# Kernel tuning notes

Measured on AMD Instinct MI355X. Metric: run time of the kernel, lower is better.

## Reference

```python
import jax, jax.numpy as jnp
import numpy as np

NUM_HEADS = 16


def setup_inputs() -> dict:
    key = jax.random.key(0)
    ks = jax.random.split(key, 8)
    S, B, E, L, P = 512, 32, 1024, 16, 10
    query = jax.random.normal(ks[0], (S, B, E), dtype=jnp.float32)
    prompt_ids = jax.random.randint(ks[1], (B, 1), 0, P, dtype=jnp.int32)
    batch_weight = jax.random.uniform(ks[2], (B,), dtype=jnp.float32)
    # xavier_uniform-like init for in_proj_weight
    bound = float(np.sqrt(6.0 / (3 * E + E)))
    in_proj_weight = jax.random.uniform(ks[3], (3 * E, E), minval=-bound, maxval=bound, dtype=jnp.float32)
    in_proj_bias = jnp.zeros((3 * E,), dtype=jnp.float32)
    ob = float(np.sqrt(6.0 / (E + E)))
    out_proj_weight = jax.random.uniform(ks[4], (E, E), minval=-ob, maxval=ob, dtype=jnp.float32)
    out_proj_bias = jnp.zeros((E,), dtype=jnp.float32)
    # prefix_pool: K-half uniform(-1,1), V-half zeros (as in torch init)
    pk = jax.random.uniform(ks[5], (P, 1, L, E), minval=-1.0, maxval=1.0, dtype=jnp.float32)
    prefix_pool = jnp.concatenate([pk, jnp.zeros((P, 1, L, E), dtype=jnp.float32)], axis=1)
    return {
        "query": query,
        "prompt_ids": prompt_ids,
        "batch_weight": batch_weight,
        "in_proj_weight": in_proj_weight,
        "in_proj_bias": in_proj_bias,
        "out_proj_weight": out_proj_weight,
        "out_proj_bias": out_proj_bias,
        "prefix_pool": prefix_pool,
    }


def _sdpa(q, k, v, scale):
    # q: [B,H,S,D], k/v: [B,H,T,D]
    scores = jnp.einsum("bhsd,bhtd->bhst", q, k) * scale
    probs = jax.nn.softmax(scores, axis=-1)
    return jnp.einsum("bhst,bhtd->bhsd", probs, v)


def reference(query, prompt_ids, batch_weight, in_proj_weight, in_proj_bias,
              out_proj_weight, out_proj_bias, prefix_pool):
    S, B, E = query.shape
    H = NUM_HEADS
    D = E // H
    scale = 1.0 / jnp.sqrt(jnp.asarray(D, dtype=query.dtype))

    # packed in-projection (q is k is v)
    qkv = query @ in_proj_weight.T + in_proj_bias          # [S,B,3E]
    q, k, v = jnp.split(qkv, 3, axis=-1)
    to_bhsd = lambda t: t.reshape(S, B, H, D).transpose(1, 2, 0, 3)  # [B,H,S,D]
    q, k, v = to_bhsd(q), to_bhsd(k), to_bhsd(v)

    # main attention
    attn = _sdpa(q, k, v, scale)                           # [B,H,S,D]

    # prefix attention
    prefix = prefix_pool[prompt_ids[:, 0]]                 # [B,2,L,E]
    L = prefix.shape[2]
    pk = prefix[:, 0].reshape(B, L, H, D).transpose(0, 2, 1, 3)  # [B,H,L,D]
    pv = prefix[:, 1].reshape(B, L, H, D).transpose(0, 2, 1, 3)
    attn_prefix = _sdpa(q, pk, pv, scale)                  # [B,H,S,D]
    attn_prefix = attn_prefix * batch_weight[:, None, None, None]

    out = attn + attn_prefix
    out = out.transpose(2, 0, 1, 3).reshape(S, B, E)       # [S,B,E]
    out = out @ out_proj_weight.T + out_proj_bias
    return out
```

## Files before the change

kernel.cpp:

```cpp
#include <hip/hip_runtime.h>
#include <stdint.h>

typedef unsigned short u16;
typedef __attribute__((ext_vector_type(8))) __bf16 bf16x8;
typedef __attribute__((ext_vector_type(4))) float f32x4;
typedef __attribute__((ext_vector_type(8))) unsigned short ushort8;

__device__ __forceinline__ u16 f2bf(float f) {
  unsigned int u = __builtin_bit_cast(unsigned int, f);
  return (u16)((u + 0x7fffu + ((u >> 16) & 1u)) >> 16);
}

__device__ __forceinline__ float fexp2(float x) {
  float r;
  asm volatile("v_exp_f32 %0, %1" : "=v"(r) : "v"(x));
  return r;
}

__device__ __forceinline__ f32x4 mfma16(bf16x8 a, bf16x8 b, f32x4 c) {
  return __builtin_amdgcn_mfma_f32_16x16x32_bf16(a, b, c, 0, 0, 0);
}

__device__ __forceinline__ void gload_lds16(const void* g, void* l) {
  __builtin_amdgcn_global_load_lds((const __attribute__((address_space(1))) void*)g,
                                   (__attribute__((address_space(3))) void*)l,
                                   16, 0, 0);
}

#define KSCALE 0.18033688011112294f

__global__ void __launch_bounds__(256) cvt_all(
    const float* __restrict__ q, const float* __restrict__ w1,
    const float* __restrict__ w2, u16* __restrict__ qb,
    u16* __restrict__ w1b, u16* __restrict__ w2b) {
  int i = blockIdx.x * 256 + threadIdx.x;
  const float* src;
  u16* dst;
  int off;
  if (i < 4194304) {
    src = q; dst = qb; off = i;
  } else if (i < 4194304 + 786432) {
    src = w1; dst = w1b; off = i - 4194304;
  } else {
    src = w2; dst = w2b; off = i - 4980736;
  }
  float4 v = ((const float4*)src)[off];
  u16* d = dst + (size_t)off * 4;
  d[0] = f2bf(v.x); d[1] = f2bf(v.y); d[2] = f2bf(v.z); d[3] = f2bf(v.w);
}

#define LDV(p) (*(const bf16x8*)(p))
#define RD_LO(AS, C) { aL[0]=LDV(AS+aRow+(C)); aL[1]=LDV(AS+aRow+1024+(C)); \
                       aL[2]=LDV(AS+aRow+2048+(C)); aL[3]=LDV(AS+aRow+3072+(C)); }
#define RD_HI(AS, C) { aH[0]=LDV(AS+aRow+4096+(C)); aH[1]=LDV(AS+aRow+5120+(C)); \
                       aH[2]=LDV(AS+aRow+6144+(C)); aH[3]=LDV(AS+aRow+7168+(C)); }
#define RD_B(BS, R, C) { R[0]=LDV(BS+bRow+(C)); R[1]=LDV(BS+bRow+1024+(C)); \
                         R[2]=LDV(BS+bRow+2048+(C)); R[3]=LDV(BS+bRow+3072+(C)); }
#define STA(DST, Q, T) gload_lds16(baseA + (Q)*K64 + (size_t)(T)*64, (DST) + (Q)*4096 + stDst)
#define STB(DST, Q, T) gload_lds16(baseB + (Q)*K64 + (size_t)(T)*64, (DST) + (Q)*4096 + stDst)
#define MM_LO(BB) { _Pragma("unroll") for (int mi=0;mi<4;++mi) \
                    _Pragma("unroll") for (int ni=0;ni<4;++ni) \
                      acc[mi][ni]=mfma16(aL[mi],(BB)[ni],acc[mi][ni]); }
#define MM_HI(BB) { _Pragma("unroll") for (int mi=0;mi<4;++mi) \
                    _Pragma("unroll") for (int ni=0;ni<4;++ni) \
                      acc[mi+4][ni]=mfma16(aH[mi],(BB)[ni],acc[mi+4][ni]); }
#define VMW(N) asm volatile("s_waitcnt vmcnt(" #N ")" ::: "memory")
#define BAR() __builtin_amdgcn_s_barrier()
#define PRIO1() __builtin_amdgcn_s_setprio(1)
#define PRIO0() __builtin_amdgcn_s_setprio(0)
#define MFMA_PH(MM, BB) { PRIO1(); MM(BB); PRIO0(); }

template <int MODE>
__global__ void __launch_bounds__(512, 2) gemm8p(
    const u16* __restrict__ A, const u16* __restrict__ B,
    const float* __restrict__ bias, void* __restrict__ Cout,
    u16* __restrict__ q_out, u16* __restrict__ k_out, u16* __restrict__ v_out,
    int M, int N, int K) {
  __shared__ alignas(16) u16 As[2][16384];
  __shared__ alignas(16) u16 Bs[2][16384];

  const int tid = threadIdx.x;
  const int w = tid >> 6, l = tid & 63;
  const int wm = w >> 2, wn = w & 3;
  const long bm = (long)blockIdx.x * 256;
  const long bn = (long)blockIdx.y * 256;
  const int NT = K >> 6;
  const int NIT = NT >> 1;

  const int srow = w * 8 + (l >> 3);
  const int schk = ((l & 7) ^ (l >> 3)) * 8;
  const u16* baseA = A + (bm + srow) * (size_t)K + schk;
  const u16* baseB = B + (bn + srow) * (size_t)K + schk;
  const size_t K64 = (size_t)K * 64;
  const int stDst = w * 512;

  u16* const as0 = &As[0][0]; u16* const as1 = &As[1][0];
  u16* const bs0 = &Bs[0][0]; u16* const bs1 = &Bs[1][0];

  const int fr = l & 15, fkg = l >> 4;
  const int sw = (fr & 7) << 3;
  const int c0 = (fkg * 8) ^ sw;
  const int c1 = (32 + fkg * 8) ^ sw;
  const int aRow = (wm * 128 + fr) * 64;
  const int bRow = (wn * 64 + fr) * 64;

  f32x4 acc[8][4] = {};
  bf16x8 aL[4], aH[4], b0[4], b1[4];

  STB(bs0, 0, 0); STB(bs0, 1, 0);
  STB(bs0, 2, 0); STB(bs0, 3, 0);
  STA(as0, 0, 0); STA(as0, 2, 0);
  STA(as0, 1, 0); STA(as0, 3, 0);
  STB(bs1, 0, 1); STB(bs1, 1, 1);
  VMW(4); BAR();

  for (int it = 0; it < NIT - 1; ++it) {
    const int t1 = 2 * it + 1, t2 = 2 * it + 2, t3 = 2 * it + 3;
    RD_LO(as0, c0); RD_B(bs0, b0, c0);
    STB(bs1, 2, t1); STB(bs1, 3, t1);
    VMW(4); BAR(); MFMA_PH(MM_LO, b0); BAR();
    RD_HI(as0, c0);
    STA(as1, 0, t1); STA(as1, 2, t1);
    BAR(); MFMA_PH(MM_HI, b0); BAR();
    RD_LO(as0, c1); RD_B(bs0, b1, c1);
    STA(as1, 1, t1); STA(as1, 3, t1);
    BAR(); MFMA_PH(MM_LO, b1); BAR();
    RD_HI(as0, c1);
    STB(bs0, 0, t2); STB(bs0, 1, t2);
    VMW(4); BAR(); MFMA_PH(MM_HI, b1); BAR();
    RD_LO(as1, c0); RD_B(bs1, b0, c0);
    STB(bs0, 2, t2); STB(bs0, 3, t2);
    VMW(4); BAR(); MFMA_PH(MM_LO, b0); BAR();
    RD_HI(as1, c0);
    STA(as0, 0, t2); STA(as0, 2, t2);
    BAR(); MFMA_PH(MM_HI, b0); BAR();
    RD_LO(as1, c1); RD_B(bs1, b1, c1);
    STA(as0, 1, t2); STA(as0, 3, t2);
    BAR(); MFMA_PH(MM_LO, b1); BAR();
    RD_HI(as1, c1);
    STB(bs1, 0, t3); STB(bs1, 1, t3);
    VMW(4); BAR(); MFMA_PH(MM_HI, b1); BAR();
  }
  {
    const int t1 = NT - 1;
    RD_LO(as0, c0); RD_B(bs0, b0, c0);
    STB(bs1, 2, t1); STB(bs1, 3, t1);
    VMW(4); BAR(); MFMA_PH(MM_LO, b0); BAR();
    RD_HI(as0, c0);
    STA(as1, 0, t1); STA(as1, 2, t1);
    BAR(); MFMA_PH(MM_HI, b0); BAR();
    RD_LO(as0, c1); RD_B(bs0, b1, c1);
    STA(as1, 1, t1); STA(as1, 3, t1);
    BAR(); MFMA_PH(MM_LO, b1); BAR();
    RD_HI(as0, c1);
    VMW(2); BAR(); MFMA_PH(MM_HI, b1); BAR();
    RD_LO(as1, c0); RD_B(bs1, b0, c0);
    VMW(0); BAR(); MFMA_PH(MM_LO, b0); BAR();
    RD_HI(as1, c0);
    BAR(); MFMA_PH(MM_HI, b0); BAR();
    RD_LO(as1, c1); RD_B(bs1, b1, c1);
    BAR(); MFMA_PH(MM_LO, b1); BAR();
    RD_HI(as1, c1);
    BAR(); MFMA_PH(MM_HI, b1);
  }

  const int r0 = wm * 128 + ((l >> 4) << 2);
  const int cc0 = wn * 64 + (l & 15);
#pragma unroll
  for (int mi = 0; mi < 8; ++mi) {
#pragma unroll
    for (int j = 0; j < 4; ++j) {
      long r = bm + r0 + mi * 16 + j;
#pragma unroll
      for (int ni = 0; ni < 4; ++ni) {
        long c = bn + cc0 + ni * 16;
        float v = acc[mi][ni][j] + bias[c];
        if (MODE == 0) {
          ((float*)Cout)[r * N + c] = v;
        } else {
          int s = (int)(r >> 5), bb = (int)(r & 31);
          int sec = (int)(c >> 10), e = (int)(c & 1023);
          int hh = e >> 6, d = e & 63;
          if (sec == 0) v *= KSCALE;
          u16* dst = (sec == 0) ? q_out : (sec == 1) ? k_out : v_out;
          dst[(((size_t)(bb * 16 + hh) * 512 + s) * 64) + d] = f2bf(v);
        }
      }
    }
  }
}

__global__ void __launch_bounds__(1024, 4) attn_v4(
    const u16* __restrict__ Q, const u16* __restrict__ K, const u16* __restrict__ V,
    const float* __restrict__ prefix_pool, const int* __restrict__ prompt_ids,
    const float* __restrict__ batch_weight, u16* __restrict__ attn_out) {
  constexpr int E = 1024, L = 16;
  const int h = blockIdx.x, b = blockIdx.y;
  const int tid = threadIdx.x;
  const int wid = tid >> 6, lane = tid & 63;
  const int fr = lane & 15, fkg = lane >> 4;

  __shared__ alignas(16) u16 Ks[64 * 64];
  __shared__ alignas(16) u16 VTs[64 * 64];
  __shared__ alignas(16) u16 Ps[16][16 * 64];
  __shared__ alignas(16) u16 pKs[L * 64];
  __shared__ alignas(16) u16 pVTs[64 * 32];

  const size_t bh = (size_t)(b * 16 + h);
  const u16* Kbase = K + bh * 512 * 64;
  const u16* Vbase = V + bh * 512 * 64;
  const u16* Qbase = Q + bh * 512 * 64;
  const int q0 = wid * 32;

  const bool isK = (tid < 512);
  const int st = isK ? tid : tid - 512;
  const int srow = st >> 3;
  const int scol = (st & 7) * 8;
  const u16* sbase = (isK ? Kbase : Vbase) + srow * 64 + scol;

  ushort8 stgA, stgB;
  stgA = *(const ushort8*)(sbase);

  const int pid = prompt_ids[b];
  const float* pk = prefix_pool + ((size_t)pid * 2 * L) * E + h * 64;
  const float* pv = pk + (size_t)L * E;
  if (tid < 256) {
    int ll = tid >> 4, d0 = (tid & 15) * 4;
    float4 v = *(const float4*)(pk + (size_t)ll * E + d0);
    u16 t4[4] = {f2bf(v.x), f2bf(v.y), f2bf(v.z), f2bf(v.w)};
#pragma unroll
    for (int i = 0; i < 4; ++i)
      pKs[(ll * 64 + d0 + i) ^ ((ll & 7) << 3)] = t4[i];
  } else if (tid < 512) {
    int t = tid - 256;
    int d = t >> 2, kv0 = (t & 3) * 8;
#pragma unroll
    for (int i = 0; i < 8; ++i) {
      int kv = kv0 + i;
      float v = (kv < L) ? pv[(size_t)kv * E + d] : 0.f;
      pVTs[d * 32 + kv] = f2bf(v);
    }
  }

  bf16x8 qf[2][2];
#pragma unroll
  for (int mt = 0; mt < 2; ++mt) {
    int qrow = q0 + mt * 16 + fr;
    qf[mt][0] = *(const bf16x8*)(Qbase + qrow * 64 + fkg * 8);
    qf[mt][1] = *(const bf16x8*)(Qbase + qrow * 64 + 32 + fkg * 8);
  }

  float m2[2] = {-3e38f, -3e38f}, lsum[2] = {0.f, 0.f};
  f32x4 oacc[2][4] = {};
  u16* const pw = Ps[wid];
  const int psw = (fr & 7) << 3;

#define STAGE_WRITE(STG)                                                      \
  if (isK) {                                                                  \
    int e = (srow * 64 + scol) ^ ((srow & 7) << 3);                           \
    *(ushort8*)(Ks + e) = STG;                                                \
  } else {                                                                    \
    _Pragma("unroll") for (int i = 0; i < 8; ++i) {                           \
      int d = scol + i;                                                       \
      VTs[(d * 64 + srow) ^ ((d & 7) << 3)] = STG[i];                         \
    }                                                                         \
  }

#define COMPUTE(CC)                                                           \
  _Pragma("unroll") for (int mt = 0; mt < 2; ++mt) {                          \
    f32x4 sa[4];                                                              \
    _Pragma("unroll") for (int nt = 0; nt < 4; ++nt) {                        \
      int krow = nt * 16 + fr;                                                \
      int kb = krow * 64, swz = (krow & 7) << 3;                              \
      bf16x8 kf0 = *(const bf16x8*)(Ks + ((kb + fkg * 8) ^ swz));             \
      bf16x8 kf1 = *(const bf16x8*)(Ks + ((kb + 32 + fkg * 8) ^ swz));        \
      f32x4 z = {};                                                           \
      sa[nt] = mfma16(kf0, qf[mt][0], z);                                     \
      sa[nt] = mfma16(kf1, qf[mt][1], sa[nt]);                                \
    }                                                                         \
    float mx = sa[0][0];                                                      \
    _Pragma("unroll") for (int nt = 0; nt < 4; ++nt)                          \
      _Pragma("unroll") for (int j = 0; j < 4; ++j)                           \
        mx = fmaxf(mx, sa[nt][j]);                                            \
    mx = fmaxf(mx, __shfl_xor(mx, 16, 64));                                   \
    mx = fmaxf(mx, __shfl_xor(mx, 32, 64));                                   \
    if (!__all(mx <= m2[mt] + 8.0f)) {                                        \
      float mnew = fmaxf(m2[mt], mx);                                         \
      float al = fexp2(m2[mt] - mnew);                                        \
      lsum[mt] *= al;                                                         \
      _Pragma("unroll") for (int j = 0; j < 4; ++j) {                         \
        float alj = __shfl(al, fkg * 4 + j, 64);                              \
        _Pragma("unroll") for (int t = 0; t < 4; ++t) oacc[mt][t][j] *= alj;  \
      }                                                                       \
      m2[mt] = mnew;                                                          \
    }                                                                         \
    float sum = 0.f;                                                          \
    _Pragma("unroll") for (int nt = 0; nt < 4; ++nt)                          \
      _Pragma("unroll") for (int j = 0; j < 4; ++j) {                         \
        float p = fexp2(sa[nt][j] - m2[mt]);                                  \
        sa[nt][j] = p;                                                        \
        sum += p;                                                             \
      }                                                                       \
    sum += __shfl_xor(sum, 16, 64);                                           \
    sum += __shfl_xor(sum, 32, 64);                                           \
    lsum[mt] += sum;                                                          \
    _Pragma("unroll") for (int nt = 0; nt < 4; ++nt)                          \
      _Pragma("unroll") for (int i = 0; i < 2; ++i) {                         \
        unsigned int pack = (unsigned int)f2bf(sa[nt][2 * i]) |               \
                            ((unsigned int)f2bf(sa[nt][2 * i + 1]) << 16);    \
        int kv = nt * 16 + fkg * 4 + 2 * i;                                   \
        *(unsigned int*)(pw + fr * 64 + (kv ^ psw)) = pack;                   \
      }                                                                       \
    _Pragma("unroll") for (int kk = 0; kk < 2; ++kk) {                        \
      bf16x8 pa = *(const bf16x8*)(pw + fr * 64 + ((kk * 32 + fkg * 8) ^ psw)); \
      _Pragma("unroll") for (int t = 0; t < 4; ++t) {                         \
        int vd = t * 16 + fr;                                                 \
        bf16x8 vf = *(const bf16x8*)(VTs + ((vd * 64 + kk * 32 + fkg * 8) ^ ((vd & 7) << 3))); \
        oacc[mt][t] = mfma16(pa, vf, oacc[mt][t]);                            \
      }                                                                       \
    }                                                                         \
  }

#define CHUNK(CUR, NXT, C)                                                    \
  {                                                                           \
    STAGE_WRITE(CUR);                                                         \
    if ((C) < 7) NXT = *(const ushort8*)(sbase + ((C) + 1) * 4096);           \
    __syncthreads();                                                          \
    COMPUTE(C);                                                               \
    __syncthreads();                                                          \
  }

  CHUNK(stgA, stgB, 0);
  CHUNK(stgB, stgA, 1);
  CHUNK(stgA, stgB, 2);
  CHUNK(stgB, stgA, 3);
  CHUNK(stgA, stgB, 4);
  CHUNK(stgB, stgA, 5);
  CHUNK(stgA, stgB, 6);
  CHUNK(stgB, stgA, 7);

  const float bw = batch_weight[b];
#pragma unroll
  for (int mt = 0; mt < 2; ++mt) {
    f32x4 sp;
    {
      int swz = (fr & 7) << 3;
      bf16x8 a0 = *(const bf16x8*)(pKs + ((fr * 64 + fkg * 8) ^ swz));
      bf16x8 a1 = *(const bf16x8*)(pKs + ((fr * 64 + 32 + fkg * 8) ^ swz));
      f32x4 z = {};
      sp = mfma16(a0, qf[mt][0], z);
      sp = mfma16(a1, qf[mt][1], sp);
    }
    float mx = fmaxf(fmaxf(sp[0], sp[1]), fmaxf(sp[2], sp[3]));
    mx = fmaxf(mx, __shfl_xor(mx, 16, 64));
    mx = fmaxf(mx, __shfl_xor(mx, 32, 64));
    float psum = 0.f;
#pragma unroll
    for (int j = 0; j < 4; ++j) {
      float p = fexp2(sp[j] - mx);
      sp[j] = p;
      psum += p;
    }
    psum += __shfl_xor(psum, 16, 64);
    psum += __shfl_xor(psum, 32, 64);
#pragma unroll
    for (int i = 0; i < 2; ++i) {
      unsigned int pack = (unsigned int)f2bf(sp[2 * i]) |
                          ((unsigned int)f2bf(sp[2 * i + 1]) << 16);
      int kv = fkg * 4 + 2 * i;
      *(unsigned int*)(pw + fr * 64 + (kv ^ psw)) = pack;
      int kv2 = 16 + fkg * 4 + 2 * i;
      *(unsigned int*)(pw + fr * 64 + (kv2 ^ psw)) = 0u;
    }
    f32x4 op[4] = {};
    {
      bf16x8 pa = *(const bf16x8*)(pw + fr * 64 + ((fkg * 8) ^ psw));
#pragma unroll
      for (int t = 0; t < 4; ++t) {
        bf16x8 vf = *(const bf16x8*)(pVTs + (t * 16 + fr) * 32 + fkg * 8);
        op[t] = mfma16(pa, vf, op[t]);
      }
    }
#pragma unroll
    for (int j = 0; j < 4; ++j) {
      float lj = __shfl(lsum[mt], fkg * 4 + j, 64);
      float lpj = __shfl(psum, fkg * 4 + j, 64);
      int s = q0 + mt * 16 + fkg * 4 + j;
      size_t m = (size_t)s * 32 + b;
      float invl = 1.f / lj, invlp = 1.f / lpj;
#pragma unroll
      for (int t = 0; t < 4; ++t) {
        float v = oacc[mt][t][j] * invl + bw * op[t][j] * invlp;
        attn_out[m * E + h * 64 + t * 16 + fr] = f2bf(v);
      }
    }
  }
}

extern "C" void kernel_launch(void* const* d_in, const int* in_sizes, int n_in,
                              void* d_out, int out_size, void* d_ws, size_t ws_size,
                              hipStream_t stream) {
  const float* query = (const float*)d_in[0];
  const int* prompt_ids = (const int*)d_in[1];
  const float* batch_weight = (const float*)d_in[2];
  const float* in_proj_w = (const float*)d_in[3];
  const float* in_proj_b = (const float*)d_in[4];
  const float* out_proj_w = (const float*)d_in[5];
  const float* out_proj_b = (const float*)d_in[6];
  const float* prefix_pool = (const float*)d_in[7];
  float* out = (float*)d_out;

  u16* qbf = (u16*)d_ws;
  u16* wqkv = qbf + (size_t)16384 * 1024;
  u16* wout = wqkv + (size_t)3072 * 1024;
  u16* qx = wout + (size_t)1024 * 1024;
  u16* kx = qx + (size_t)32 * 16 * 512 * 64;
  u16* vx = kx + (size_t)32 * 16 * 512 * 64;
  u16* attnb = vx + (size_t)32 * 16 * 512 * 64;

  cvt_all<<<20480, 256, 0, stream>>>(query, in_proj_w, out_proj_w,
                                     qbf, wqkv, wout);

  gemm8p<2><<<dim3(64, 12), 512, 0, stream>>>(qbf, wqkv, in_proj_b, nullptr,
                                              qx, kx, vx, 16384, 3072, 1024);
  attn_v4<<<dim3(16, 32), 1024, 0, stream>>>(qx, kx, vx, prefix_pool, prompt_ids,
                                             batch_weight, attnb);
  gemm8p<0><<<dim3(64, 4), 512, 0, stream>>>(attnb, wout, out_proj_b, out,
                                             nullptr, nullptr, nullptr,
                                             16384, 1024, 1024);
}
```

Measured before the change: 245.5 us.

## Stage QKV epilogue through LDS for vectorized head-major stores and retime loads

The QKV projection epilogue now writes bf16 results into the shared-memory tile (swizzled), then each thread emits 16-byte vector stores into the [B,H,S,D] q/k/v layouts instead of scattered 2-byte stores. The per-section branch is hoisted since each 256-column block lies in one section. The main-loop load schedule is also reordered, issuing all A loads for the next tile earlier and changing the vmcnt waits, with a trailing barrier so the tile buffer can be reused. This trades extra LDS traffic and a sync for far fewer, coalesced global writes, and it shifts the prefetch timing, which may affect overlap.

Result: slower. 256.9 us (+4.7%).

```diff
diff --git a/kernel.cpp b/kernel.cpp
--- a/kernel.cpp
+++ b/kernel.cpp
@@ -76,8 +76,7 @@
     const float* __restrict__ bias, void* __restrict__ Cout,
     u16* __restrict__ q_out, u16* __restrict__ k_out, u16* __restrict__ v_out,
     int M, int N, int K) {
-  __shared__ alignas(16) u16 As[2][16384];
-  __shared__ alignas(16) u16 Bs[2][16384];
+  __shared__ alignas(16) u16 SH[65536];
 
   const int tid = threadIdx.x;
   const int w = tid >> 6, l = tid & 63;
@@ -94,8 +93,10 @@
   const size_t K64 = (size_t)K * 64;
   const int stDst = w * 512;
 
-  u16* const as0 = &As[0][0]; u16* const as1 = &As[1][0];
-  u16* const bs0 = &Bs[0][0]; u16* const bs1 = &Bs[1][0];
+  u16* const as0 = SH;
+  u16* const as1 = SH + 16384;
+  u16* const bs0 = SH + 32768;
+  u16* const bs1 = SH + 49152;
 
   const int fr = l & 15, fkg = l >> 4;
   const int sw = (fr & 7) << 3;
@@ -107,85 +108,111 @@
   f32x4 acc[8][4] = {};
   bf16x8 aL[4], aH[4], b0[4], b1[4];
 
-  STB(bs0, 0, 0); STB(bs0, 1, 0);
-  STB(bs0, 2, 0); STB(bs0, 3, 0);
-  STA(as0, 0, 0); STA(as0, 2, 0);
-  STA(as0, 1, 0); STA(as0, 3, 0);
+  STB(bs0, 0, 0); STB(bs0, 1, 0); STB(bs0, 2, 0); STB(bs0, 3, 0);
+  STA(as0, 0, 0); STA(as0, 1, 0); STA(as0, 2, 0); STA(as0, 3, 0);
   STB(bs1, 0, 1); STB(bs1, 1, 1);
-  VMW(4); BAR();
+  VMW(2); BAR();
 
   for (int it = 0; it < NIT - 1; ++it) {
     const int t1 = 2 * it + 1, t2 = 2 * it + 2, t3 = 2 * it + 3;
     RD_LO(as0, c0); RD_B(bs0, b0, c0);
+    STA(as1, 0, t1); STA(as1, 2, t1); STA(as1, 1, t1); STA(as1, 3, t1);
     STB(bs1, 2, t1); STB(bs1, 3, t1);
-    VMW(4); BAR(); MFMA_PH(MM_LO, b0); BAR();
+    BAR(); MFMA_PH(MM_LO, b0); BAR();
     RD_HI(as0, c0);
-    STA(as1, 0, t1); STA(as1, 2, t1);
     BAR(); MFMA_PH(MM_HI, b0); BAR();
     RD_LO(as0, c1); RD_B(bs0, b1, c1);
-    STA(as1, 1, t1); STA(as1, 3, t1);
     BAR(); MFMA_PH(MM_LO, b1); BAR();
     RD_HI(as0, c1);
-    STB(bs0, 0, t2); STB(bs0, 1, t2);
-    VMW(4); BAR(); MFMA_PH(MM_HI, b1); BAR();
+    STB(bs0, 0, t2); STB(bs0, 1, t2); STB(bs0, 2, t2); STB(bs0, 3, t2);
+    VMW(4);
+    BAR(); MFMA_PH(MM_HI, b1); BAR();
     RD_LO(as1, c0); RD_B(bs1, b0, c0);
-    STB(bs0, 2, t2); STB(bs0, 3, t2);
-    VMW(4); BAR(); MFMA_PH(MM_LO, b0); BAR();
+    STA(as0, 0, t2); STA(as0, 2, t2);
+    BAR(); MFMA_PH(MM_LO, b0); BAR();
     RD_HI(as1, c0);
-    STA(as0, 0, t2); STA(as0, 2, t2);
+    STA(as0, 1, t2); STA(as0, 3, t2);
     BAR(); MFMA_PH(MM_HI, b0); BAR();
     RD_LO(as1, c1); RD_B(bs1, b1, c1);
-    STA(as0, 1, t2); STA(as0, 3, t2);
     BAR(); MFMA_PH(MM_LO, b1); BAR();
     RD_HI(as1, c1);
     STB(bs1, 0, t3); STB(bs1, 1, t3);
-    VMW(4); BAR(); MFMA_PH(MM_HI, b1); BAR();
-  }
+    VMW(2);
+    BAR(); MFMA_PH(MM_HI, b1); BAR();
+  }
+
   {
     const int t1 = NT - 1;
     RD_LO(as0, c0); RD_B(bs0, b0, c0);
+    STA(as1, 0, t1); STA(as1, 2, t1); STA(as1, 1, t1); STA(as1, 3, t1);
     STB(bs1, 2, t1); STB(bs1, 3, t1);
-    VMW(4); BAR(); MFMA_PH(MM_LO, b0); BAR();
+    BAR(); MFMA_PH(MM_LO, b0); BAR();
     RD_HI(as0, c0);
-    STA(as1, 0, t1); STA(as1, 2, t1);
     BAR(); MFMA_PH(MM_HI, b0); BAR();
     RD_LO(as0, c1); RD_B(bs0, b1, c1);
-    STA(as1, 1, t1); STA(as1, 3, t1);
     BAR(); MFMA_PH(MM_LO, b1); BAR();
     RD_HI(as0, c1);
-    VMW(2); BAR(); MFMA_PH(MM_HI, b1); BAR();
+    VMW(0);
+    BAR(); MFMA_PH(MM_HI, b1); BAR();
     RD_LO(as1, c0); RD_B(bs1, b0, c0);
-    VMW(0); BAR(); MFMA_PH(MM_LO, b0); BAR();
+    BAR(); MFMA_PH(MM_LO, b0); BAR();
     RD_HI(as1, c0);
     BAR(); MFMA_PH(MM_HI, b0); BAR();
     RD_LO(as1, c1); RD_B(bs1, b1, c1);
     BAR(); MFMA_PH(MM_LO, b1); BAR();
     RD_HI(as1, c1);
     BAR(); MFMA_PH(MM_HI, b1);
-  }
-
-  const int r0 = wm * 128 + ((l >> 4) << 2);
-  const int cc0 = wn * 64 + (l & 15);
-#pragma unroll
-  for (int mi = 0; mi < 8; ++mi) {
-#pragma unroll
-    for (int j = 0; j < 4; ++j) {
-      long r = bm + r0 + mi * 16 + j;
-#pragma unroll
-      for (int ni = 0; ni < 4; ++ni) {
-        long c = bn + cc0 + ni * 16;
-        float v = acc[mi][ni][j] + bias[c];
-        if (MODE == 0) {
-          ((float*)Cout)[r * N + c] = v;
-        } else {
-          int s = (int)(r >> 5), bb = (int)(r & 31);
-          int sec = (int)(c >> 10), e = (int)(c & 1023);
-          int hh = e >> 6, d = e & 63;
-          if (sec == 0) v *= KSCALE;
-          u16* dst = (sec == 0) ? q_out : (sec == 1) ? k_out : v_out;
-          dst[(((size_t)(bb * 16 + hh) * 512 + s) * 64) + d] = f2bf(v);
+    BAR();
+  }
+
+  if (MODE == 0) {
+    const int r0 = wm * 128 + ((l >> 4) << 2);
+    const int cc0 = wn * 64 + (l & 15);
+#pragma unroll
+    for (int mi = 0; mi < 8; ++mi) {
+#pragma unroll
+      for (int j = 0; j < 4; ++j) {
+        long r = bm + r0 + mi * 16 + j;
+#pragma unroll
+        for (int ni = 0; ni < 4; ++ni) {
+          long c = bn + cc0 + ni * 16;
+          ((float*)Cout)[r * N + c] = acc[mi][ni][j] + bias[c];
         }
       }
+    }
+  } else {
+    const int sec = (int)(bn >> 10);
+    const float kmul = (sec == 0) ? KSCALE : 1.0f;
+    const int colBase = wn * 64 + (l & 15);
+    const int rowBase = wm * 128 + ((l >> 4) << 2);
+#pragma unroll
+    for (int mi = 0; mi < 8; ++mi) {
+#pragma unroll
+      for (int j = 0; j < 4; ++j) {
+        int row = rowBase + mi * 16 + j;
+        int rsw = ((row >> 1) & 7) << 3;
+#pragma unroll
+        for (int ni = 0; ni < 4; ++ni) {
+          int col = colBase + ni * 16;
+          float v = (acc[mi][ni][j] + bias[bn + col]) * kmul;
+          SH[row * 256 + (col ^ rsw)] = f2bf(v);
+        }
+      }
+    }
+    __syncthreads();
+    u16* const dst = (sec == 0) ? q_out : (sec == 1) ? k_out : v_out;
+    const int ebase = (int)(bn & 1023);
+#pragma unroll
+    for (int k = 0; k < 16; ++k) {
+      int s5 = tid + 512 * k;
+      int row = s5 >> 5;
+      int col = (s5 & 31) * 8;
+      ushort8 v = *(const ushort8*)(SH + row * 256 + (col ^ (((row >> 1) & 7) << 3)));
+      long r = bm + row;
+      int s = (int)(r >> 5), bb = (int)(r & 31);
+      int e = ebase + col;
+      int hh = e >> 6, d0 = e & 63;
+      *(ushort8*)(dst + (((size_t)(bb * 16 + hh) * 512 + s) * 64) + d0) = v;
     }
   }
 }
```
